# Kernel tuning notes

Hardware: AMD Instinct MI355X
Metric: run time of the kernel (lower is better)

Reference implementation:

```python
import jax, jax.numpy as jnp
import numpy as np

B, S, D = 2, 4096, 1024
H, HD = 16, 64
M = 512              # memseqlen == chunk size
L = 2 * M            # memory + chunk tokens
HID = 2816
EPS = 1e-5


def setup_inputs() -> dict:
    key = jax.random.key(0)
    ks = jax.random.split(key, 16)
    sc = 0.02
    return {
        "x": jax.random.normal(ks[0], (B, S, D), jnp.float32),
        "freqs_cos": jax.random.uniform(ks[1], (L, HD // 2), jnp.float32),
        "freqs_sin": jax.random.uniform(ks[2], (L, HD // 2), jnp.float32),
        "wq": jax.random.normal(ks[3], (D, D), jnp.float32) * sc,
        "wk": jax.random.normal(ks[4], (D, D), jnp.float32) * sc,
        "wv": jax.random.normal(ks[5], (D, D), jnp.float32) * sc,
        "wo": jax.random.normal(ks[6], (D, D), jnp.float32) * sc,
        "wm": jax.random.normal(ks[7], (D, D), jnp.float32) * sc,
        "wkm": jax.random.normal(ks[8], (D, D), jnp.float32) * sc,
        "wvm": jax.random.normal(ks[9], (D, D), jnp.float32) * sc,
        "w1": jax.random.normal(ks[10], (D, HID), jnp.float32) * sc,
        "w3": jax.random.normal(ks[11], (D, HID), jnp.float32) * sc,
        "w2": jax.random.normal(ks[12], (HID, D), jnp.float32) * sc,
        "ffn_norm_w": jnp.ones((D,), jnp.float32),
        "mem_norm_w": jnp.ones((D,), jnp.float32),
        "origin_mem": jnp.zeros((1, M, D), jnp.float32),
    }


def _rmsnorm(x, w):
    return x * jax.lax.rsqrt(jnp.mean(x * x, axis=-1, keepdims=True) + EPS) * w


def _rope(t, cos, sin):
    # t: (B, L, H, HD); cos/sin: (L, HD//2). Adjacent-pair complex rotation (llama2.c style).
    tr = t.reshape(*t.shape[:-1], HD // 2, 2)
    t_r, t_i = tr[..., 0], tr[..., 1]
    c = cos[None, :, None, :]
    s = sin[None, :, None, :]
    o_r = t_r * c - t_i * s
    o_i = t_r * s + t_i * c
    return jnp.stack([o_r, o_i], axis=-1).reshape(t.shape)


def reference(x, freqs_cos, freqs_sin, wq, wk, wv, wo, wm, wkm, wvm,
              w1, w2, w3, ffn_norm_w, mem_norm_w, origin_mem):
    bsz = x.shape[0]
    cos = freqs_cos[:L]
    sin = freqs_sin[:L]
    causal = jnp.tril(jnp.ones((L, L), dtype=bool))
    scale = 1.0 / jnp.sqrt(jnp.asarray(HD, x.dtype))

    def ffn(h):
        return (jax.nn.silu(h @ w1) * (h @ w3)) @ w2

    def step(om, subx):
        # token projections
        xq = (subx @ wq).reshape(bsz, M, H, HD)
        xk = (subx @ wk).reshape(bsz, M, H, HD)
        xv = (subx @ wv).reshape(bsz, M, H, HD)
        # memory glue: wm -> ffn residual -> rmsnorm
        om2 = om @ wm
        om2 = om2 + ffn(_rmsnorm(om2, ffn_norm_w))
        om2 = _rmsnorm(om2, mem_norm_w)
        # memory projections (source bug: mq is overwritten by mk; wqm unused)
        mk = (om2 @ wkm).reshape(bsz, M, H, HD)
        mv = (om2 @ wvm).reshape(bsz, M, H, HD)
        mq = mk
        q = jnp.concatenate([mq, xq], axis=1)  # (B, L, H, HD)
        k = jnp.concatenate([mk, xk], axis=1)
        v = jnp.concatenate([mv, xv], axis=1)
        q = _rope(q, cos, sin)
        k = _rope(k, cos, sin)
        # SDPA, causal over the concatenated length (n_rep == 1, repeat_kv is identity)
        qh = q.transpose(0, 2, 1, 3)
        kh = k.transpose(0, 2, 1, 3)
        vh = v.transpose(0, 2, 1, 3)
        scores = jnp.einsum('bhqd,bhkd->bhqk', qh, kh) * scale
        scores = jnp.where(causal, scores, jnp.finfo(scores.dtype).min)
        attn = jax.nn.softmax(scores, axis=-1)
        out = jnp.einsum('bhqk,bhkd->bhqd', attn, vh)
        out = out.transpose(0, 2, 1, 3).reshape(bsz, L, D)
        om_new = out[:, M:]  # token-part becomes next memory AND this chunk's output
        return om_new, om_new

    om0 = jnp.broadcast_to(origin_mem, (bsz, M, D))
    xc = x.reshape(bsz, S // M, M, D).transpose(1, 0, 2, 3)  # (n_chunks, B, M, D)
    _, outs = jax.lax.scan(step, om0, xc)
    out = outs.transpose(1, 0, 2, 3).reshape(bsz, S, D)
    return out @ wo
```

## Files before the change

kernel.cpp:

```cpp
#include <hip/hip_runtime.h>
#include <hip/hip_bf16.h>


#define D_    1024
#define H_    16
#define HD_   64
#define M_    512
#define L_    1024
#define HID_  2816
#define NSTEP 8

typedef __hip_bfloat16 bf16;
typedef _Float16 f16;
typedef __attribute__((ext_vector_type(8))) short short8;
typedef __attribute__((ext_vector_type(8))) _Float16 f16x8;
typedef __attribute__((ext_vector_type(2))) _Float16 f16x2;
typedef __attribute__((ext_vector_type(4))) float floatx4;

__global__ void probe_dtype(const void* x, int* flag) {
  int lane = threadIdx.x;
  unsigned short v = ((const unsigned short*)x)[2 * lane];
  int e = (v >> 7) & 0xFF;
  bool sane = (e >= 100 && e <= 140);
  unsigned long long m = __ballot(sane);
  if (lane == 0) flag[0] = (__popcll(m) >= 40) ? 1 : 0;
}

__device__ __forceinline__ float load_any(const void* p, long i, int isbf) {
  return isbf ? __bfloat162float(((const bf16*)p)[i]) : ((const float*)p)[i];
}

__global__ __launch_bounds__(256) void transpose_cast(const void* in, bf16* out,
                                                      int K, int N, const int* flagp,
                                                      int stride, int off) {
  __shared__ float tile[32][33];
  int isbf = flagp[0];
  int tx = threadIdx.x & 31, ty = threadIdx.x >> 5;
  int n = blockIdx.x * 32 + tx;
#pragma unroll
  for (int i = 0; i < 4; i++) {
    int k = blockIdx.y * 32 + ty + i * 8;
    tile[ty + i * 8][tx] = load_any(in, (long)k * N + n, isbf);
  }
  __syncthreads();
  int k2 = blockIdx.y * 32 + tx;
#pragma unroll
  for (int i = 0; i < 4; i++) {
    int n2 = blockIdx.x * 32 + ty + i * 8;
    out[((long)n2 * stride + off) * K + k2] = __float2bfloat16(tile[tx][ty + i * 8]);
  }
}

__global__ __launch_bounds__(256) void cast_to_bf16(const void* in, bf16* out, int n,
                                                    const int* flagp) {
  int i = blockIdx.x * 256 + threadIdx.x;
  if (i < n) out[i] = __float2bfloat16(load_any(in, i, flagp[0]));
}

__global__ __launch_bounds__(256) void cast_to_f32(const void* in, float* out, int n,
                                                   const int* flagp) {
  int i = blockIdx.x * 256 + threadIdx.x;
  if (i < n) out[i] = load_any(in, i, flagp[0]);
}

__global__ __launch_bounds__(256) void init_om(const void* in, bf16* om, const int* flagp) {
  int i = blockIdx.x * 256 + threadIdx.x;
  int rem = i & (M_ * D_ - 1);
  om[i] = __float2bfloat16(load_any(in, rem, flagp[0]));
}

__global__ __launch_bounds__(256) void gemm64(
    const bf16* __restrict__ A, const bf16* __restrict__ WT,
    void* __restrict__ out, const int* __restrict__ flagp,
    int N, int K, int out_mode) {
  __shared__ char smem[16384];
  char* aT = smem;
  char* bT = smem + 8192;
  int tid = threadIdx.x;
  int C0 = blockIdx.x * 64, R0 = blockIdx.y * 64;
  int wave = tid >> 6, lane = tid & 63;
  int wm_ = wave >> 1, wn_ = wave & 1;
  floatx4 acc[2][2] = {};

  int q0 = tid, q1 = tid + 256;
  int am0 = q0 >> 3, ac0 = q0 & 7;
  int am1 = q1 >> 3, ac1 = q1 & 7;
  long grow0 = R0 + am0, grow1 = R0 + am1;
  long bn0 = (long)(C0 + am0) * K, bn1 = (long)(C0 + am1) * K;
  int lofa0 = (am0 * 8 + (ac0 ^ (am0 & 7))) * 16;
  int lofa1 = (am1 * 8 + (ac1 ^ (am1 & 7))) * 16;

  for (int k0 = 0; k0 < K; k0 += 64) {
    uint4 va0 = *(const uint4*)(A + grow0 * K + k0 + ac0 * 8);
    uint4 va1 = *(const uint4*)(A + grow1 * K + k0 + ac1 * 8);
    uint4 vb0 = *(const uint4*)(WT + bn0 + k0 + ac0 * 8);
    uint4 vb1 = *(const uint4*)(WT + bn1 + k0 + ac1 * 8);
    __syncthreads();
    *(uint4*)(aT + lofa0) = va0;
    *(uint4*)(aT + lofa1) = va1;
    *(uint4*)(bT + lofa0) = vb0;
    *(uint4*)(bT + lofa1) = vb1;
    __syncthreads();
#pragma unroll
    for (int kki = 0; kki < 2; ++kki) {
      int cbase = kki * 4 + (lane >> 4);
      short8 af[2], bfr[2];
#pragma unroll
      for (int i = 0; i < 2; ++i) {
        int ml = wm_ * 32 + i * 16 + (lane & 15);
        af[i] = *(const short8*)(aT + (ml * 8 + (cbase ^ (ml & 7))) * 16);
        int nl = wn_ * 32 + i * 16 + (lane & 15);
        bfr[i] = *(const short8*)(bT + (nl * 8 + (cbase ^ (nl & 7))) * 16);
      }
#pragma unroll
      for (int i = 0; i < 2; ++i)
#pragma unroll
        for (int j = 0; j < 2; ++j)
          acc[i][j] = __builtin_amdgcn_mfma_f32_16x16x32_bf16(af[i], bfr[j], acc[i][j], 0, 0, 0);
    }
  }
  int isbf = flagp[0];
#pragma unroll
  for (int i = 0; i < 2; ++i)
#pragma unroll
    for (int j = 0; j < 2; ++j) {
      int row = R0 + wm_ * 32 + i * 16 + (lane >> 4) * 4;
      int col = C0 + wn_ * 32 + j * 16 + (lane & 15);
#pragma unroll
      for (int rg = 0; rg < 4; ++rg) {
        float v = acc[i][j][rg];
        long off = (long)(row + rg) * N + col;
        if (out_mode == 0) ((float*)out)[off] = v;
        else if (out_mode == 1) ((f16*)out)[off] = (f16)v;
        else {
          if (isbf) ((bf16*)out)[off] = __float2bfloat16(v);
          else ((float*)out)[off] = v;
        }
      }
    }
}

__global__ __launch_bounds__(256) void gemm64_sk(
    const bf16* __restrict__ A, const bf16* __restrict__ WT,
    float* __restrict__ out0, float* __restrict__ out1,
    int N, int Kfull, int Ksplit) {
  __shared__ char smem[16384];
  char* aT = smem;
  char* bT = smem + 8192;
  int tid = threadIdx.x;
  int C0 = blockIdx.x * 64, R0 = blockIdx.y * 64;
  int kb = blockIdx.z;
  float* out = kb ? out1 : out0;
  int kbeg = kb * Ksplit, kend = kbeg + Ksplit;
  int wave = tid >> 6, lane = tid & 63;
  int wm_ = wave >> 1, wn_ = wave & 1;
  floatx4 acc[2][2] = {};

  int q0 = tid, q1 = tid + 256;
  int am0 = q0 >> 3, ac0 = q0 & 7;
  int am1 = q1 >> 3, ac1 = q1 & 7;
  long grow0 = R0 + am0, grow1 = R0 + am1;
  long bn0 = (long)(C0 + am0) * Kfull, bn1 = (long)(C0 + am1) * Kfull;
  int lofa0 = (am0 * 8 + (ac0 ^ (am0 & 7))) * 16;
  int lofa1 = (am1 * 8 + (ac1 ^ (am1 & 7))) * 16;

  for (int k0 = kbeg; k0 < kend; k0 += 64) {
    uint4 va0 = *(const uint4*)(A + grow0 * Kfull + k0 + ac0 * 8);
    uint4 va1 = *(const uint4*)(A + grow1 * Kfull + k0 + ac1 * 8);
    uint4 vb0 = *(const uint4*)(WT + bn0 + k0 + ac0 * 8);
    uint4 vb1 = *(const uint4*)(WT + bn1 + k0 + ac1 * 8);
    __syncthreads();
    *(uint4*)(aT + lofa0) = va0;
    *(uint4*)(aT + lofa1) = va1;
    *(uint4*)(bT + lofa0) = vb0;
    *(uint4*)(bT + lofa1) = vb1;
    __syncthreads();
#pragma unroll
    for (int kki = 0; kki < 2; ++kki) {
      int cbase = kki * 4 + (lane >> 4);
      short8 af[2], bfr[2];
#pragma unroll
      for (int i = 0; i < 2; ++i) {
        int ml = wm_ * 32 + i * 16 + (lane & 15);
        af[i] = *(const short8*)(aT + (ml * 8 + (cbase ^ (ml & 7))) * 16);
        int nl = wn_ * 32 + i * 16 + (lane & 15);
        bfr[i] = *(const short8*)(bT + (nl * 8 + (cbase ^ (nl & 7))) * 16);
      }
#pragma unroll
      for (int i = 0; i < 2; ++i)
#pragma unroll
        for (int j = 0; j < 2; ++j)
          acc[i][j] = __builtin_amdgcn_mfma_f32_16x16x32_bf16(af[i], bfr[j], acc[i][j], 0, 0, 0);
    }
  }
#pragma unroll
  for (int i = 0; i < 2; ++i)
#pragma unroll
    for (int j = 0; j < 2; ++j) {
      int row = R0 + wm_ * 32 + i * 16 + (lane >> 4) * 4;
      int col = C0 + wn_ * 32 + j * 16 + (lane & 15);
#pragma unroll
      for (int rg = 0; rg < 4; ++rg)
        out[(long)(row + rg) * N + col] = acc[i][j][rg];
    }
}

__global__ __launch_bounds__(256) void gemm128(
    const bf16* __restrict__ A, const bf16* __restrict__ WT,
    void* __restrict__ out, const int* __restrict__ flagp,
    int N, int K, int out_mode) {
  __shared__ char smem[32768];
  int tid = threadIdx.x;
  int w = tid >> 6, lane = tid & 63;
  int C0 = blockIdx.x * 128, R0 = blockIdx.y * 128;
  int wm = (w >> 1) * 64, wn = (w & 1) * 64;
  int g = lane >> 4, n16 = lane & 15;
  floatx4 acc[4][4] = {};
  int lr = lane >> 3, lc = lane & 7;

  for (int k0 = 0; k0 < K; k0 += 64) {
    __syncthreads();
#pragma unroll
    for (int i = 0; i < 4; ++i) {
      int m = w * 32 + i * 8 + lr;
      int cg = lc ^ (m & 7);
      const bf16* ga = A + (size_t)(R0 + m) * K + k0 + cg * 8;
      const bf16* gb = WT + (size_t)(C0 + m) * K + k0 + cg * 8;
      __builtin_amdgcn_global_load_lds(
          (const __attribute__((address_space(1))) void*)ga,
          (__attribute__((address_space(3))) void*)(smem + (w * 32 + i * 8) * 128),
          16, 0, 0);
      __builtin_amdgcn_global_load_lds(
          (const __attribute__((address_space(1))) void*)gb,
          (__attribute__((address_space(3))) void*)(smem + 16384 + (w * 32 + i * 8) * 128),
          16, 0, 0);
    }
    __syncthreads();
#pragma unroll
    for (int kk = 0; kk < 2; ++kk) {
      short8 af[4], bfr[4];
#pragma unroll
      for (int i = 0; i < 4; ++i) {
        int ml = wm + i * 16 + n16;
        af[i] = *(const short8*)(smem + (ml * 8 + ((kk * 4 + g) ^ (ml & 7))) * 16);
        int nl = wn + i * 16 + n16;
        bfr[i] = *(const short8*)(smem + 16384 + (nl * 8 + ((kk * 4 + g) ^ (nl & 7))) * 16);
      }
#pragma unroll
      for (int i = 0; i < 4; ++i)
#pragma unroll
        for (int j = 0; j < 4; ++j)
          acc[i][j] = __builtin_amdgcn_mfma_f32_16x16x32_bf16(af[i], bfr[j], acc[i][j], 0, 0, 0);
    }
  }
  int isbf = flagp[0];
#pragma unroll
  for (int i = 0; i < 4; ++i)
#pragma unroll
    for (int j = 0; j < 4; ++j) {
      int row = R0 + wm + i * 16 + g * 4;
      int col = C0 + wn + j * 16 + n16;
#pragma unroll
      for (int rg = 0; rg < 4; ++rg) {
        float v = acc[i][j][rg];
        if (out_mode == 3) {
          float partner = __shfl_xor(v, 1);
          if ((n16 & 1) == 0) {
            float a = v;
            float s = a / (1.f + __expf(-a));
            ((bf16*)out)[(long)(row + rg) * HID_ + (col >> 1)] =
                __float2bfloat16(s * partner);
          }
          continue;
        }
        long off = (long)(row + rg) * N + col;
        if (out_mode == 0) ((float*)out)[off] = v;
        else if (out_mode == 1) ((f16*)out)[off] = (f16)v;
        else {
          if (isbf) ((bf16*)out)[off] = __float2bfloat16(v);
          else ((float*)out)[off] = v;
        }
      }
    }
}

__global__ __launch_bounds__(256) void rmsnorm_cast(const float* __restrict__ X,
                                                    const float* __restrict__ Wn,
                                                    bf16* __restrict__ Y,
                                                    const float* __restrict__ X1,
                                                    const float* __restrict__ X2,
                                                    float* __restrict__ sumout) {
  int row = blockIdx.x, tid = threadIdx.x;
  const float* xr = X + (long)row * D_;
  float vals[4], ss = 0.f;
#pragma unroll
  for (int i = 0; i < 4; i++) {
    int c = tid + i * 256;
    float v = xr[c];
    if (X1) v += X1[(long)row * D_ + c];
    if (X2) v += X2[(long)row * D_ + c];
    vals[i] = v;
    ss += v * v;
  }
#pragma unroll
  for (int off = 32; off; off >>= 1) ss += __shfl_xor(ss, off);
  __shared__ float wsum[4];
  int wv = tid >> 6, lane = tid & 63;
  if (lane == 0) wsum[wv] = ss;
  __syncthreads();
  ss = wsum[0] + wsum[1] + wsum[2] + wsum[3];
  float r = rsqrtf(ss * (1.0f / D_) + 1e-5f);
#pragma unroll
  for (int i = 0; i < 4; i++) {
    int c = tid + i * 256;
    if (sumout) sumout[(long)row * D_ + c] = vals[i];
    Y[(long)row * D_ + c] = __float2bfloat16(vals[i] * r * Wn[c]);
  }
}

__global__ __launch_bounds__(256) void rope_x(
    const f16* __restrict__ qkv, const float* __restrict__ cosf,
    const float* __restrict__ sinf, f16* __restrict__ q_x,
    f16* __restrict__ k_x, f16* __restrict__ v_xT) {
  __shared__ f16 tile[64][72];
  int pt = blockIdx.x;
  int t = blockIdx.y;
  int bh = blockIdx.z;
  int b = bh >> 4, h = bh & 15;
  int tid = threadIdx.x;
  int i = tid & 31, p0 = tid >> 5;
  size_t slab = (size_t)t * 32 + bh;
#pragma unroll
  for (int j = 0; j < 8; ++j) {
    int pl = p0 + j * 8;
    int m = pt * 64 + pl;
    int pos = 512 + m;
    long base = ((long)b * 4096 + t * 512 + m) * 3072 + h * 64 + 2 * i;
    float c = cosf[pos * 32 + i], s = sinf[pos * 32 + i];
    float q0 = (float)qkv[base], q1 = (float)qkv[base + 1];
    f16x2 qw; qw.x = (f16)((q0 * c - q1 * s) * 0.125f);
    qw.y = (f16)((q0 * s + q1 * c) * 0.125f);
    *(f16x2*)(q_x + (slab * 512 + m) * 64 + 2 * i) = qw;
    float k0 = (float)qkv[base + 1024], k1 = (float)qkv[base + 1025];
    f16x2 kw; kw.x = (f16)(k0 * c - k1 * s); kw.y = (f16)(k0 * s + k1 * c);
    *(f16x2*)(k_x + (slab * 512 + m) * 64 + 2 * i) = kw;
    tile[2 * i][pl] = qkv[base + 2048];
    tile[2 * i + 1][pl] = qkv[base + 2049];
  }
  __syncthreads();
#pragma unroll
  for (int j = 0; j < 8; ++j) {
    int d = p0 + j * 8;
    f16x2 vv; vv.x = tile[d][2 * i]; vv.y = tile[d][2 * i + 1];
    *(f16x2*)(v_xT + (slab * 64 + d) * 512 + pt * 64 + 2 * i) = vv;
  }
}

__global__ __launch_bounds__(256) void rope_mem(
    const f16* __restrict__ mkv, const float* __restrict__ cosf,
    const float* __restrict__ sinf, f16* __restrict__ k_mem,
    f16* __restrict__ v_memT) {
  __shared__ f16 tile[64][72];
  int pt = blockIdx.x;
  int bh = blockIdx.y;
  int b = bh >> 4, h = bh & 15;
  int tid = threadIdx.x;
  int i = tid & 31, p0 = tid >> 5;
#pragma unroll
  for (int j = 0; j < 8; ++j) {
    int pl = p0 + j * 8;
    int pos = pt * 64 + pl;
    long base = ((long)(b * 512 + pos)) * 2048 + h * 64 + 2 * i;
    float c = cosf[pos * 32 + i], s = sinf[pos * 32 + i];
    float k0 = (float)mkv[base], k1 = (float)mkv[base + 1];
    f16x2 kw; kw.x = (f16)(k0 * c - k1 * s); kw.y = (f16)(k0 * s + k1 * c);
    *(f16x2*)(k_mem + ((size_t)bh * 512 + pos) * 64 + 2 * i) = kw;
    tile[2 * i][pl] = mkv[base + 1024];
    tile[2 * i + 1][pl] = mkv[base + 1025];
  }
  __syncthreads();
#pragma unroll
  for (int j = 0; j < 8; ++j) {
    int d = p0 + j * 8;
    f16x2 vv; vv.x = tile[d][2 * i]; vv.y = tile[d][2 * i + 1];
    *(f16x2*)(v_memT + ((size_t)bh * 64 + d) * 512 + pt * 64 + 2 * i) = vv;
  }
}

__global__ __launch_bounds__(256) void attn_mfma(
    const f16* __restrict__ q_x, const f16* __restrict__ k_mem,
    const f16* __restrict__ v_memT, const f16* __restrict__ k_x,
    const f16* __restrict__ v_xT, bf16* __restrict__ om_bf,
    bf16* __restrict__ outs_bf, int t) {
  __shared__ char smem[24576];
  int qt = blockIdx.x, bh = blockIdx.y;
  int tid = threadIdx.x;
  int w = tid >> 6, lane = tid & 63;
  int g = lane >> 4, n16 = lane & 15;
  int numc = 9 + qt;
  int pos = 512 + qt * 64 + w * 16 + n16;
  size_t slab = (size_t)t * 32 + bh;

  f16x8 qf[2];
  {
    const f16* qp = q_x + (slab * 512 + qt * 64 + w * 16 + n16) * 64 + g * 8;
    qf[0] = *(const f16x8*)(qp);
    qf[1] = *(const f16x8*)(qp + 32);
  }
  floatx4 O[4] = {};
  float mrun = -1e30f, lrun = 0.f;

  int id0 = tid, id1 = tid + 256;
  int r0 = id0 >> 3, c0 = id0 & 7;
  int r1 = id1 >> 3, c1 = id1 & 7;
  int lof0 = ((r0 << 3) | (c0 ^ (r0 & 7))) * 16;
  int lof1 = ((r1 << 3) | (c1 ^ (r1 & 7))) * 16;

  auto kaddr = [&](int c, int r) -> const f16* {
    return (c < 8) ? k_mem + ((size_t)bh * 512 + c * 64 + r) * 64
                   : k_x + (slab * 512 + (c - 8) * 64 + r) * 64;
  };
  auto vaddr = [&](int c, int d) -> const f16* {
    return (c < 8) ? v_memT + ((size_t)bh * 64 + d) * 512 + c * 64
                   : v_xT + (slab * 64 + d) * 512 + (c - 8) * 64;
  };

  uint4 kv0 = *(const uint4*)(kaddr(0, r0) + c0 * 8);
  uint4 kv1 = *(const uint4*)(kaddr(0, r1) + c1 * 8);
  uint4 vv0 = *(const uint4*)(vaddr(0, r0) + c0 * 8);
  uint4 vv1 = *(const uint4*)(vaddr(0, r1) + c1 * 8);

  char* Pw = smem + 16384 + w * 2048;

  for (int c = 0; c < numc; ++c) {
    __syncthreads();
    *(uint4*)(smem + lof0) = kv0;
    *(uint4*)(smem + lof1) = kv1;
    *(uint4*)(smem + 8192 + lof0) = vv0;
    *(uint4*)(smem + 8192 + lof1) = vv1;
    if (c + 1 < numc) {
      kv0 = *(const uint4*)(kaddr(c + 1, r0) + c0 * 8);
      kv1 = *(const uint4*)(kaddr(c + 1, r1) + c1 * 8);
      vv0 = *(const uint4*)(vaddr(c + 1, r0) + c0 * 8);
      vv1 = *(const uint4*)(vaddr(c + 1, r1) + c1 * 8);
    }
    __syncthreads();

    floatx4 S[4] = {};
#pragma unroll
    for (int kk = 0; kk < 2; ++kk) {
#pragma unroll
      for (int tn = 0; tn < 4; ++tn) {
        int row = tn * 16 + n16;
        f16x8 kf = *(const f16x8*)(smem + (((row << 3) | ((kk * 4 + g) ^ (row & 7))) * 16));
        S[tn] = __builtin_amdgcn_mfma_f32_16x16x32_f16(kf, qf[kk], S[tn], 0, 0, 0);
      }
    }
    if (c == numc - 1) {
      int kb = 512 + (c - 8) * 64;
#pragma unroll
      for (int tn = 0; tn < 4; ++tn)
#pragma unroll
        for (int r = 0; r < 4; ++r) {
          int key = kb + tn * 16 + g * 4 + r;
          if (key > pos) S[tn][r] = -1e30f;
        }
    }
    float smax = -1e30f;
#pragma unroll
    for (int tn = 0; tn < 4; ++tn)
#pragma unroll
      for (int r = 0; r < 4; ++r) smax = fmaxf(smax, S[tn][r]);
    smax = fmaxf(smax, __shfl_xor(smax, 16));
    smax = fmaxf(smax, __shfl_xor(smax, 32));
    float newm = fmaxf(mrun, smax);
    float corr = __expf(mrun - newm);
    mrun = newm;
    float lsum = 0.f;
    f16 pv[16];
#pragma unroll
    for (int tn = 0; tn < 4; ++tn)
#pragma unroll
      for (int r = 0; r < 4; ++r) {
        float p = __expf(S[tn][r] - newm);
        lsum += p;
        pv[tn * 4 + r] = (f16)p;
      }
    lsum += __shfl_xor(lsum, 16);
    lsum += __shfl_xor(lsum, 32);
    lrun = lrun * corr + lsum;
    float cr[4];
#pragma unroll
    for (int r = 0; r < 4; ++r) cr[r] = __shfl(corr, g * 4 + r);
#pragma unroll
    for (int dt = 0; dt < 4; ++dt)
#pragma unroll
      for (int r = 0; r < 4; ++r) O[dt][r] *= cr[r];
#pragma unroll
    for (int tn = 0; tn < 4; ++tn)
#pragma unroll
      for (int r = 0; r < 4; ++r) {
        int kap = tn * 16 + g * 4 + r;
        *(f16*)(Pw + (((n16 << 3) | ((kap >> 3) ^ (n16 & 7))) * 16 + (kap & 7) * 2)) =
            pv[tn * 4 + r];
      }
#pragma unroll
    for (int kk = 0; kk < 2; ++kk) {
      f16x8 pf = *(const f16x8*)(Pw + (((n16 << 3) | ((kk * 4 + g) ^ (n16 & 7))) * 16));
#pragma unroll
      for (int dt = 0; dt < 4; ++dt) {
        int row = dt * 16 + n16;
        f16x8 vf =
            *(const f16x8*)(smem + 8192 + (((row << 3) | ((kk * 4 + g) ^ (row & 7))) * 16));
        O[dt] = __builtin_amdgcn_mfma_f32_16x16x32_f16(pf, vf, O[dt], 0, 0, 0);
      }
    }
  }
  float rl = 1.0f / lrun;
  float rlr[4];
#pragma unroll
  for (int r = 0; r < 4; ++r) rlr[r] = __shfl(rl, g * 4 + r);
  int b = bh >> 4, h = bh & 15;
#pragma unroll
  for (int dt = 0; dt < 4; ++dt)
#pragma unroll
    for (int r = 0; r < 4; ++r) {
      int qq = qt * 64 + w * 16 + g * 4 + r;
      bf16 v = __float2bfloat16(O[dt][r] * rlr[r]);
      size_t col = h * 64 + dt * 16 + n16;
      om_bf[((size_t)(b * 512 + qq)) * 1024 + col] = v;
      outs_bf[((size_t)(b * 4096 + t * 512 + qq)) * 1024 + col] = v;
    }
}

extern "C" void kernel_launch(void* const* d_in, const int* in_sizes, int n_in,
                              void* d_out, int out_size, void* d_ws, size_t ws_size,
                              hipStream_t stream) {
  (void)in_sizes; (void)n_in; (void)out_size; (void)ws_size;
  const void* x   = d_in[0];
  const void* fc  = d_in[1];
  const void* fs  = d_in[2];
  const void* wq  = d_in[3];
  const void* wk  = d_in[4];
  const void* wv  = d_in[5];
  const void* wo  = d_in[6];
  const void* wm  = d_in[7];
  const void* wkm = d_in[8];
  const void* wvm = d_in[9];
  const void* w1  = d_in[10];
  const void* w3  = d_in[11];
  const void* w2  = d_in[12];
  const void* fnw = d_in[13];
  const void* mnw = d_in[14];
  const void* om0 = d_in[15];

  char* p = (char*)d_ws;
  auto alloc = [&](size_t bytes) -> char* {
    char* r = p;
    p += (bytes + 255) & ~(size_t)255;
    return r;
  };
  int*   flag    = (int*)alloc(256);
  bf16*  wqkvT   = (bf16*)alloc((size_t)3 * 1048576 * 2);
  bf16*  wmT     = (bf16*)alloc((size_t)1048576 * 2);
  bf16*  wkmvmT  = (bf16*)alloc((size_t)2 * 1048576 * 2);
  bf16*  w13T    = (bf16*)alloc((size_t)2 * 2883584 * 2);
  bf16*  w2T     = (bf16*)alloc((size_t)2883584 * 2);
  bf16*  woT     = (bf16*)alloc((size_t)1048576 * 2);
  bf16*  xb      = (bf16*)alloc((size_t)8388608 * 2);
  float* cosf    = (float*)alloc((size_t)32768 * 4);
  float* sinf    = (float*)alloc((size_t)32768 * 4);
  float* ffnw    = (float*)alloc((size_t)1024 * 4);
  float* memw    = (float*)alloc((size_t)1024 * 4);
  bf16*  om_bf   = (bf16*)alloc((size_t)1048576 * 2);
  bf16*  outs_bf = (bf16*)alloc((size_t)8388608 * 2);
  f16*   q_x     = (f16*)alloc((size_t)8 * 32 * 512 * 64 * 2);
  f16*   k_x     = (f16*)alloc((size_t)8 * 32 * 512 * 64 * 2);
  f16*   v_xT    = (f16*)alloc((size_t)8 * 32 * 512 * 64 * 2);
  char*  shr     = alloc((size_t)8192 * 3072 * 2);
  f16*   qkvf_all = (f16*)shr;
  char*  lp = shr;
  auto lalloc = [&](size_t bytes) -> char* {
    char* r = lp;
    lp += (bytes + 255) & ~(size_t)255;
    return r;
  };
  float* om2a   = (float*)lalloc((size_t)1048576 * 4);
  bf16*  h_bf   = (bf16*)lalloc((size_t)1048576 * 2);
  bf16*  u_bf   = (bf16*)lalloc((size_t)2883584 * 2);
  float* fbuf   = (float*)lalloc((size_t)1048576 * 4);
  float* fbuf2  = (float*)lalloc((size_t)1048576 * 4);
  bf16*  om2_bf = (bf16*)lalloc((size_t)1048576 * 2);
  f16*   mkv    = (f16*)lalloc((size_t)2097152 * 2);
  f16*   k_mem  = (f16*)lalloc((size_t)1048576 * 2);
  f16*   v_memT = (f16*)lalloc((size_t)1048576 * 2);

  dim3 tb(256);
  probe_dtype<<<1, 64, 0, stream>>>(x, flag);

  transpose_cast<<<dim3(32, 32), tb, 0, stream>>>(wq, wqkvT, 1024, 1024, flag, 1, 0);
  transpose_cast<<<dim3(32, 32), tb, 0, stream>>>(wk, wqkvT + 1048576, 1024, 1024, flag, 1, 0);
  transpose_cast<<<dim3(32, 32), tb, 0, stream>>>(wv, wqkvT + 2 * 1048576, 1024, 1024, flag, 1, 0);
  transpose_cast<<<dim3(32, 32), tb, 0, stream>>>(wm, wmT, 1024, 1024, flag, 1, 0);
  transpose_cast<<<dim3(32, 32), tb, 0, stream>>>(wkm, wkmvmT, 1024, 1024, flag, 1, 0);
  transpose_cast<<<dim3(32, 32), tb, 0, stream>>>(wvm, wkmvmT + 1048576, 1024, 1024, flag, 1, 0);
  transpose_cast<<<dim3(88, 32), tb, 0, stream>>>(w1, w13T, 1024, 2816, flag, 2, 0);
  transpose_cast<<<dim3(88, 32), tb, 0, stream>>>(w3, w13T, 1024, 2816, flag, 2, 1);
  transpose_cast<<<dim3(32, 88), tb, 0, stream>>>(w2, w2T, 2816, 1024, flag, 1, 0);
  transpose_cast<<<dim3(32, 32), tb, 0, stream>>>(wo, woT, 1024, 1024, flag, 1, 0);

  cast_to_bf16<<<32768, tb, 0, stream>>>(x, xb, 8388608, flag);
  cast_to_f32<<<128, tb, 0, stream>>>(fc, cosf, 32768, flag);
  cast_to_f32<<<128, tb, 0, stream>>>(fs, sinf, 32768, flag);
  cast_to_f32<<<4, tb, 0, stream>>>(fnw, ffnw, 1024, flag);
  cast_to_f32<<<4, tb, 0, stream>>>(mnw, memw, 1024, flag);
  init_om<<<4096, tb, 0, stream>>>(om0, om_bf, flag);

  gemm128<<<dim3(24, 64), tb, 0, stream>>>(xb, wqkvT, qkvf_all, flag, 3072, 1024, 1);
  rope_x<<<dim3(8, 8, 32), tb, 0, stream>>>(qkvf_all, cosf, sinf, q_x, k_x, v_xT);

  for (int t = 0; t < NSTEP; ++t) {
    gemm64_sk<<<dim3(16, 16, 2), tb, 0, stream>>>(om_bf, wmT, om2a, fbuf, 1024, 1024, 512);
    rmsnorm_cast<<<1024, tb, 0, stream>>>(om2a, ffnw, h_bf, fbuf, nullptr, om2a);
    gemm128<<<dim3(44, 8), tb, 0, stream>>>(h_bf, w13T, u_bf, flag, 5632, 1024, 3);
    gemm64_sk<<<dim3(16, 16, 2), tb, 0, stream>>>(u_bf, w2T, fbuf, fbuf2, 1024, 2816, 1408);
    rmsnorm_cast<<<1024, tb, 0, stream>>>(om2a, memw, om2_bf, fbuf, fbuf2, nullptr);
    gemm64<<<dim3(32, 16), tb, 0, stream>>>(om2_bf, wkmvmT, mkv, flag, 2048, 1024, 1);
    rope_mem<<<dim3(8, 32), tb, 0, stream>>>(mkv, cosf, sinf, k_mem, v_memT);
    attn_mfma<<<dim3(8, 32), tb, 0, stream>>>(q_x, k_mem, v_memT, k_x, v_xT,
                                              om_bf, outs_bf, t);
  }
  gemm128<<<dim3(8, 64), tb, 0, stream>>>(outs_bf, woT, d_out, flag, 1024, 1024, 2);
}
```

Before: 1.150 ms.

## Split attention over memory/token keys, fuse RoPE into KV GEMM, swizzle tiles

Attention is split along the key axis into a memory part and a token part, run as two blocks per query tile, and merged by a new kernel that combines the partial softmax statistics. This doubles the number of attention workgroups so a small grid fills more of the GPU. RoPE and the V transpose are folded into the memory K/V GEMM epilogue, which removes the separate rope_mem pass and its intermediate buffer. gemm128 gains an XCD-style block-index swizzle, and s_setprio is raised around the MFMA sections. The cost is an extra fp32 partial-output round trip and one more launch per step.

```diff
diff --git a/kernel.cpp b/kernel.cpp
--- a/kernel.cpp
+++ b/kernel.cpp
@@ -69,56 +69,54 @@
   om[i] = __float2bfloat16(load_any(in, rem, flagp[0]));
 }
 
+#define GEMM64_BODY(Aptr, WTptr, Kld, kbeg, kend)                                   \
+  __shared__ char smem[16384];                                                      \
+  char* aT = smem;                                                                  \
+  char* bT = smem + 8192;                                                           \
+  int tid = threadIdx.x;                                                            \
+  int wave = tid >> 6, lane = tid & 63;                                             \
+  int wm_ = wave >> 1, wn_ = wave & 1;                                              \
+  floatx4 acc[2][2] = {};                                                           \
+  int q0 = tid, q1 = tid + 256;                                                     \
+  int am0 = q0 >> 3, ac0 = q0 & 7;                                                  \
+  int am1 = q1 >> 3, ac1 = q1 & 7;                                                  \
+  long grow0 = R0 + am0, grow1 = R0 + am1;                                          \
+  long bn0 = (long)(C0 + am0) * (Kld), bn1 = (long)(C0 + am1) * (Kld);              \
+  int lofa0 = (am0 * 8 + (ac0 ^ (am0 & 7))) * 16;                                   \
+  int lofa1 = (am1 * 8 + (ac1 ^ (am1 & 7))) * 16;                                   \
+  for (int k0 = (kbeg); k0 < (kend); k0 += 64) {                                    \
+    uint4 va0 = *(const uint4*)((Aptr) + grow0 * (Kld) + k0 + ac0 * 8);             \
+    uint4 va1 = *(const uint4*)((Aptr) + grow1 * (Kld) + k0 + ac1 * 8);             \
+    uint4 vb0 = *(const uint4*)((WTptr) + bn0 + k0 + ac0 * 8);                      \
+    uint4 vb1 = *(const uint4*)((WTptr) + bn1 + k0 + ac1 * 8);                      \
+    __syncthreads();                                                                \
+    *(uint4*)(aT + lofa0) = va0;                                                    \
+    *(uint4*)(aT + lofa1) = va1;                                                    \
+    *(uint4*)(bT + lofa0) = vb0;                                                    \
+    *(uint4*)(bT + lofa1) = vb1;                                                    \
+    __syncthreads();                                                                \
+    _Pragma("unroll") for (int kki = 0; kki < 2; ++kki) {                           \
+      int cbase = kki * 4 + (lane >> 4);                                            \
+      short8 af[2], bfr[2];                                                         \
+      _Pragma("unroll") for (int i = 0; i < 2; ++i) {                               \
+        int ml = wm_ * 32 + i * 16 + (lane & 15);                                   \
+        af[i] = *(const short8*)(aT + (ml * 8 + (cbase ^ (ml & 7))) * 16);          \
+        int nl = wn_ * 32 + i * 16 + (lane & 15);                                   \
+        bfr[i] = *(const short8*)(bT + (nl * 8 + (cbase ^ (nl & 7))) * 16);         \
+      }                                                                             \
+      _Pragma("unroll") for (int i = 0; i < 2; ++i)                                 \
+          _Pragma("unroll") for (int j = 0; j < 2; ++j) acc[i][j] =                 \
+              __builtin_amdgcn_mfma_f32_16x16x32_bf16(af[i], bfr[j], acc[i][j],     \
+                                                      0, 0, 0);                     \
+    }                                                                               \
+  }
+
 __global__ __launch_bounds__(256) void gemm64(
     const bf16* __restrict__ A, const bf16* __restrict__ WT,
     void* __restrict__ out, const int* __restrict__ flagp,
     int N, int K, int out_mode) {
-  __shared__ char smem[16384];
-  char* aT = smem;
-  char* bT = smem + 8192;
-  int tid = threadIdx.x;
   int C0 = blockIdx.x * 64, R0 = blockIdx.y * 64;
-  int wave = tid >> 6, lane = tid & 63;
-  int wm_ = wave >> 1, wn_ = wave & 1;
-  floatx4 acc[2][2] = {};
-
-  int q0 = tid, q1 = tid + 256;
-  int am0 = q0 >> 3, ac0 = q0 & 7;
-  int am1 = q1 >> 3, ac1 = q1 & 7;
-  long grow0 = R0 + am0, grow1 = R0 + am1;
-  long bn0 = (long)(C0 + am0) * K, bn1 = (long)(C0 + am1) * K;
-  int lofa0 = (am0 * 8 + (ac0 ^ (am0 & 7))) * 16;
-  int lofa1 = (am1 * 8 + (ac1 ^ (am1 & 7))) * 16;
-
-  for (int k0 = 0; k0 < K; k0 += 64) {
-    uint4 va0 = *(const uint4*)(A + grow0 * K + k0 + ac0 * 8);
-    uint4 va1 = *(const uint4*)(A + grow1 * K + k0 + ac1 * 8);
-    uint4 vb0 = *(const uint4*)(WT + bn0 + k0 + ac0 * 8);
-    uint4 vb1 = *(const uint4*)(WT + bn1 + k0 + ac1 * 8);
-    __syncthreads();
-    *(uint4*)(aT + lofa0) = va0;
-    *(uint4*)(aT + lofa1) = va1;
-    *(uint4*)(bT + lofa0) = vb0;
-    *(uint4*)(bT + lofa1) = vb1;
-    __syncthreads();
-#pragma unroll
-    for (int kki = 0; kki < 2; ++kki) {
-      int cbase = kki * 4 + (lane >> 4);
-      short8 af[2], bfr[2];
-#pragma unroll
-      for (int i = 0; i < 2; ++i) {
-        int ml = wm_ * 32 + i * 16 + (lane & 15);
-        af[i] = *(const short8*)(aT + (ml * 8 + (cbase ^ (ml & 7))) * 16);
-        int nl = wn_ * 32 + i * 16 + (lane & 15);
-        bfr[i] = *(const short8*)(bT + (nl * 8 + (cbase ^ (nl & 7))) * 16);
-      }
-#pragma unroll
-      for (int i = 0; i < 2; ++i)
-#pragma unroll
-        for (int j = 0; j < 2; ++j)
-          acc[i][j] = __builtin_amdgcn_mfma_f32_16x16x32_bf16(af[i], bfr[j], acc[i][j], 0, 0, 0);
-    }
-  }
+  GEMM64_BODY(A, WT, K, 0, K)
   int isbf = flagp[0];
 #pragma unroll
   for (int i = 0; i < 2; ++i)
@@ -144,55 +142,11 @@
     const bf16* __restrict__ A, const bf16* __restrict__ WT,
     float* __restrict__ out0, float* __restrict__ out1,
     int N, int Kfull, int Ksplit) {
-  __shared__ char smem[16384];
-  char* aT = smem;
-  char* bT = smem + 8192;
-  int tid = threadIdx.x;
   int C0 = blockIdx.x * 64, R0 = blockIdx.y * 64;
   int kb = blockIdx.z;
   float* out = kb ? out1 : out0;
-  int kbeg = kb * Ksplit, kend = kbeg + Ksplit;
-  int wave = tid >> 6, lane = tid & 63;
-  int wm_ = wave >> 1, wn_ = wave & 1;
-  floatx4 acc[2][2] = {};
-
-  int q0 = tid, q1 = tid + 256;
-  int am0 = q0 >> 3, ac0 = q0 & 7;
-  int am1 = q1 >> 3, ac1 = q1 & 7;
-  long grow0 = R0 + am0, grow1 = R0 + am1;
-  long bn0 = (long)(C0 + am0) * Kfull, bn1 = (long)(C0 + am1) * Kfull;
-  int lofa0 = (am0 * 8 + (ac0 ^ (am0 & 7))) * 16;
-  int lofa1 = (am1 * 8 + (ac1 ^ (am1 & 7))) * 16;
-
-  for (int k0 = kbeg; k0 < kend; k0 += 64) {
-    uint4 va0 = *(const uint4*)(A + grow0 * Kfull + k0 + ac0 * 8);
-    uint4 va1 = *(const uint4*)(A + grow1 * Kfull + k0 + ac1 * 8);
-    uint4 vb0 = *(const uint4*)(WT + bn0 + k0 + ac0 * 8);
-    uint4 vb1 = *(const uint4*)(WT + bn1 + k0 + ac1 * 8);
-    __syncthreads();
-    *(uint4*)(aT + lofa0) = va0;
-    *(uint4*)(aT + lofa1) = va1;
-    *(uint4*)(bT + lofa0) = vb0;
-    *(uint4*)(bT + lofa1) = vb1;
-    __syncthreads();
-#pragma unroll
-    for (int kki = 0; kki < 2; ++kki) {
-      int cbase = kki * 4 + (lane >> 4);
-      short8 af[2], bfr[2];
-#pragma unroll
-      for (int i = 0; i < 2; ++i) {
-        int ml = wm_ * 32 + i * 16 + (lane & 15);
-        af[i] = *(const short8*)(aT + (ml * 8 + (cbase ^ (ml & 7))) * 16);
-        int nl = wn_ * 32 + i * 16 + (lane & 15);
-        bfr[i] = *(const short8*)(bT + (nl * 8 + (cbase ^ (nl & 7))) * 16);
-      }
-#pragma unroll
-      for (int i = 0; i < 2; ++i)
-#pragma unroll
-        for (int j = 0; j < 2; ++j)
-          acc[i][j] = __builtin_amdgcn_mfma_f32_16x16x32_bf16(af[i], bfr[j], acc[i][j], 0, 0, 0);
-    }
-  }
+  int kbeg = kb * Ksplit;
+  GEMM64_BODY(A, WT, Kfull, kbeg, kbeg + Ksplit)
 #pragma unroll
   for (int i = 0; i < 2; ++i)
 #pragma unroll
@@ -202,6 +156,39 @@
 #pragma unroll
       for (int rg = 0; rg < 4; ++rg)
         out[(long)(row + rg) * N + col] = acc[i][j][rg];
+    }
+}
+
+__global__ __launch_bounds__(256) void gemm64_kmvm(
+    const bf16* __restrict__ A, const bf16* __restrict__ WT,
+    const float* __restrict__ cosf, const float* __restrict__ sinf,
+    f16* __restrict__ k_mem, f16* __restrict__ v_memT) {
+  int C0 = blockIdx.x * 64, R0 = blockIdx.y * 64;
+  GEMM64_BODY(A, WT, 1024, 0, 1024)
+#pragma unroll
+  for (int i = 0; i < 2; ++i)
+#pragma unroll
+    for (int j = 0; j < 2; ++j) {
+      int row0 = R0 + wm_ * 32 + i * 16 + (lane >> 4) * 4;
+      int col = C0 + wn_ * 32 + j * 16 + (lane & 15);
+#pragma unroll
+      for (int rg = 0; rg < 4; ++rg) {
+        float v = acc[i][j][rg];
+        int row = row0 + rg;
+        int b = row >> 9, pos = row & 511;
+        if (C0 < 1024) {
+          float partner = __shfl_xor(v, 1);
+          int ii = (col & 63) >> 1;
+          float c = cosf[pos * 32 + ii], s = sinf[pos * 32 + ii];
+          float o = (col & 1) ? (partner * s + v * c) : (v * c - partner * s);
+          int bh = b * 16 + ((col >> 6) & 15);
+          k_mem[((size_t)bh * 512 + pos) * 64 + (col & 63)] = (f16)o;
+        } else {
+          int d = col & 63;
+          int bh = b * 16 + ((col - 1024) >> 6);
+          v_memT[((size_t)bh * 64 + d) * 512 + pos] = (f16)v;
+        }
+      }
     }
 }
 
@@ -212,7 +199,17 @@
   __shared__ char smem[32768];
   int tid = threadIdx.x;
   int w = tid >> 6, lane = tid & 63;
-  int C0 = blockIdx.x * 128, R0 = blockIdx.y * 128;
+  int bx = blockIdx.x, by = blockIdx.y;
+  {
+    int nwg = gridDim.x * gridDim.y;
+    if ((nwg & 7) == 0) {
+      int lin = by * gridDim.x + bx;
+      int swz = (lin & 7) * (nwg >> 3) + (lin >> 3);
+      bx = swz % gridDim.x;
+      by = swz / gridDim.x;
+    }
+  }
+  int C0 = bx * 128, R0 = by * 128;
   int wm = (w >> 1) * 64, wn = (w & 1) * 64;
   int g = lane >> 4, n16 = lane & 15;
   floatx4 acc[4][4] = {};
@@ -356,48 +353,18 @@
   }
 }
 
-__global__ __launch_bounds__(256) void rope_mem(
-    const f16* __restrict__ mkv, const float* __restrict__ cosf,
-    const float* __restrict__ sinf, f16* __restrict__ k_mem,
-    f16* __restrict__ v_memT) {
-  __shared__ f16 tile[64][72];
-  int pt = blockIdx.x;
-  int bh = blockIdx.y;
-  int b = bh >> 4, h = bh & 15;
-  int tid = threadIdx.x;
-  int i = tid & 31, p0 = tid >> 5;
-#pragma unroll
-  for (int j = 0; j < 8; ++j) {
-    int pl = p0 + j * 8;
-    int pos = pt * 64 + pl;
-    long base = ((long)(b * 512 + pos)) * 2048 + h * 64 + 2 * i;
-    float c = cosf[pos * 32 + i], s = sinf[pos * 32 + i];
-    float k0 = (float)mkv[base], k1 = (float)mkv[base + 1];
-    f16x2 kw; kw.x = (f16)(k0 * c - k1 * s); kw.y = (f16)(k0 * s + k1 * c);
-    *(f16x2*)(k_mem + ((size_t)bh * 512 + pos) * 64 + 2 * i) = kw;
-    tile[2 * i][pl] = mkv[base + 1024];
-    tile[2 * i + 1][pl] = mkv[base + 1025];
-  }
-  __syncthreads();
-#pragma unroll
-  for (int j = 0; j < 8; ++j) {
-    int d = p0 + j * 8;
-    f16x2 vv; vv.x = tile[d][2 * i]; vv.y = tile[d][2 * i + 1];
-    *(f16x2*)(v_memT + ((size_t)bh * 64 + d) * 512 + pt * 64 + 2 * i) = vv;
-  }
-}
-
 __global__ __launch_bounds__(256) void attn_mfma(
     const f16* __restrict__ q_x, const f16* __restrict__ k_mem,
     const f16* __restrict__ v_memT, const f16* __restrict__ k_x,
-    const f16* __restrict__ v_xT, bf16* __restrict__ om_bf,
-    bf16* __restrict__ outs_bf, int t) {
+    const f16* __restrict__ v_xT, float* __restrict__ Opart,
+    float* __restrict__ mpart, float* __restrict__ lpart, int t) {
   __shared__ char smem[24576];
-  int qt = blockIdx.x, bh = blockIdx.y;
+  int qt = blockIdx.x, bh = blockIdx.y, z = blockIdx.z;
   int tid = threadIdx.x;
   int w = tid >> 6, lane = tid & 63;
   int g = lane >> 4, n16 = lane & 15;
-  int numc = 9 + qt;
+  int c0 = z ? 8 : 0;
+  int numc = z ? (qt + 1) : 8;
   int pos = 512 + qt * 64 + w * 16 + n16;
   size_t slab = (size_t)t * 32 + bh;
 
@@ -411,10 +378,10 @@
   float mrun = -1e30f, lrun = 0.f;
 
   int id0 = tid, id1 = tid + 256;
-  int r0 = id0 >> 3, c0 = id0 & 7;
-  int r1 = id1 >> 3, c1 = id1 & 7;
-  int lof0 = ((r0 << 3) | (c0 ^ (r0 & 7))) * 16;
-  int lof1 = ((r1 << 3) | (c1 ^ (r1 & 7))) * 16;
+  int r0 = id0 >> 3, cc0 = id0 & 7;
+  int r1 = id1 >> 3, cc1 = id1 & 7;
+  int lof0 = ((r0 << 3) | (cc0 ^ (r0 & 7))) * 16;
+  int lof1 = ((r1 << 3) | (cc1 ^ (r1 & 7))) * 16;
 
   auto kaddr = [&](int c, int r) -> const f16* {
     return (c < 8) ? k_mem + ((size_t)bh * 512 + c * 64 + r) * 64
@@ -425,10 +392,10 @@
                    : v_xT + (slab * 64 + d) * 512 + (c - 8) * 64;
   };
 
-  uint4 kv0 = *(const uint4*)(kaddr(0, r0) + c0 * 8);
-  uint4 kv1 = *(const uint4*)(kaddr(0, r1) + c1 * 8);
-  uint4 vv0 = *(const uint4*)(vaddr(0, r0) + c0 * 8);
-  uint4 vv1 = *(const uint4*)(vaddr(0, r1) + c1 * 8);
+  uint4 kv0 = *(const uint4*)(kaddr(c0, r0) + cc0 * 8);
+  uint4 kv1 = *(const uint4*)(kaddr(c0, r1) + cc1 * 8);
+  uint4 vv0 = *(const uint4*)(vaddr(c0, r0) + cc0 * 8);
+  uint4 vv1 = *(const uint4*)(vaddr(c0, r1) + cc1 * 8);
 
   char* Pw = smem + 16384 + w * 2048;
 
@@ -439,14 +406,15 @@
     *(uint4*)(smem + 8192 + lof0) = vv0;
     *(uint4*)(smem + 8192 + lof1) = vv1;
     if (c + 1 < numc) {
-      kv0 = *(const uint4*)(kaddr(c + 1, r0) + c0 * 8);
-      kv1 = *(const uint4*)(kaddr(c + 1, r1) + c1 * 8);
-      vv0 = *(const uint4*)(vaddr(c + 1, r0) + c0 * 8);
-      vv1 = *(const uint4*)(vaddr(c + 1, r1) + c1 * 8);
+      kv0 = *(const uint4*)(kaddr(c0 + c + 1, r0) + cc0 * 8);
+      kv1 = *(const uint4*)(kaddr(c0 + c + 1, r1) + cc1 * 8);
+      vv0 = *(const uint4*)(vaddr(c0 + c + 1, r0) + cc0 * 8);
+      vv1 = *(const uint4*)(vaddr(c0 + c + 1, r1) + cc1 * 8);
     }
     __syncthreads();
 
     floatx4 S[4] = {};
+    __builtin_amdgcn_s_setprio(1);
 #pragma unroll
     for (int kk = 0; kk < 2; ++kk) {
 #pragma unroll
@@ -456,8 +424,9 @@
         S[tn] = __builtin_amdgcn_mfma_f32_16x16x32_f16(kf, qf[kk], S[tn], 0, 0, 0);
       }
     }
-    if (c == numc - 1) {
-      int kb = 512 + (c - 8) * 64;
+    __builtin_amdgcn_s_setprio(0);
+    if (z == 1 && c == numc - 1) {
+      int kb = 512 + qt * 64;
 #pragma unroll
       for (int tn = 0; tn < 4; ++tn)
 #pragma unroll
@@ -504,6 +473,7 @@
         *(f16*)(Pw + (((n16 << 3) | ((kap >> 3) ^ (n16 & 7))) * 16 + (kap & 7) * 2)) =
             pv[tn * 4 + r];
       }
+    __builtin_amdgcn_s_setprio(1);
 #pragma unroll
     for (int kk = 0; kk < 2; ++kk) {
       f16x8 pf = *(const f16x8*)(Pw + (((n16 << 3) | ((kk * 4 + g) ^ (n16 & 7))) * 16));
@@ -515,22 +485,47 @@
         O[dt] = __builtin_amdgcn_mfma_f32_16x16x32_f16(pf, vf, O[dt], 0, 0, 0);
       }
     }
-  }
-  float rl = 1.0f / lrun;
-  float rlr[4];
-#pragma unroll
-  for (int r = 0; r < 4; ++r) rlr[r] = __shfl(rl, g * 4 + r);
+    __builtin_amdgcn_s_setprio(0);
+  }
   int b = bh >> 4, h = bh & 15;
+  if (g == 0) {
+    int qq = qt * 64 + w * 16 + n16;
+    mpart[(size_t)z * 16384 + bh * 512 + qq] = mrun;
+    lpart[(size_t)z * 16384 + bh * 512 + qq] = lrun;
+  }
 #pragma unroll
   for (int dt = 0; dt < 4; ++dt)
 #pragma unroll
     for (int r = 0; r < 4; ++r) {
       int qq = qt * 64 + w * 16 + g * 4 + r;
-      bf16 v = __float2bfloat16(O[dt][r] * rlr[r]);
-      size_t col = h * 64 + dt * 16 + n16;
-      om_bf[((size_t)(b * 512 + qq)) * 1024 + col] = v;
-      outs_bf[((size_t)(b * 4096 + t * 512 + qq)) * 1024 + col] = v;
-    }
+      size_t col = (size_t)h * 64 + dt * 16 + n16;
+      Opart[(size_t)z * 1048576 + (size_t)(b * 512 + qq) * 1024 + col] = O[dt][r];
+    }
+}
+
+__global__ __launch_bounds__(256) void attn_merge(
+    const float* __restrict__ Opart, const float* __restrict__ mpart,
+    const float* __restrict__ lpart, bf16* __restrict__ om_bf,
+    bf16* __restrict__ outs_bf, int t) {
+  int row = blockIdx.x;
+  int b = row >> 9, qq = row & 511;
+  int tid = threadIdx.x;
+#pragma unroll
+  for (int ii = 0; ii < 4; ++ii) {
+    int col = tid + ii * 256;
+    int bh = b * 16 + (col >> 6);
+    int idx = bh * 512 + qq;
+    float m1 = mpart[idx], l1 = lpart[idx];
+    float m2 = mpart[16384 + idx], l2 = lpart[16384 + idx];
+    float Mx = fmaxf(m1, m2);
+    float a1 = __expf(m1 - Mx), a2 = __expf(m2 - Mx);
+    float o1 = Opart[(size_t)row * 1024 + col];
+    float o2 = Opart[1048576 + (size_t)row * 1024 + col];
+    float v = (a1 * o1 + a2 * o2) / (a1 * l1 + a2 * l2);
+    bf16 bv = __float2bfloat16(v);
+    om_bf[(size_t)row * 1024 + col] = bv;
+    outs_bf[((size_t)(b * 4096 + t * 512 + qq)) * 1024 + col] = bv;
+  }
 }
 
 extern "C" void kernel_launch(void* const* d_in, const int* in_sizes, int n_in,
@@ -591,9 +586,11 @@
   float* fbuf   = (float*)lalloc((size_t)1048576 * 4);
   float* fbuf2  = (float*)lalloc((size_t)1048576 * 4);
   bf16*  om2_bf = (bf16*)lalloc((size_t)1048576 * 2);
-  f16*   mkv    = (f16*)lalloc((size_t)2097152 * 2);
   f16*   k_mem  = (f16*)lalloc((size_t)1048576 * 2);
   f16*   v_memT = (f16*)lalloc((size_t)1048576 * 2);
+  float* Opart  = (float*)lalloc((size_t)2 * 1048576 * 4);
+  float* mpart  = (float*)lalloc((size_t)2 * 16384 * 4);
+  float* lpart  = (float*)lalloc((size_t)2 * 16384 * 4);
 
   dim3 tb(256);
   probe_dtype<<<1, 64, 0, stream>>>(x, flag);
@@ -625,10 +622,10 @@
     gemm128<<<dim3(44, 8), tb, 0, stream>>>(h_bf, w13T, u_bf, flag, 5632, 1024, 3);
     gemm64_sk<<<dim3(16, 16, 2), tb, 0, stream>>>(u_bf, w2T, fbuf, fbuf2, 1024, 2816, 1408);
     rmsnorm_cast<<<1024, tb, 0, stream>>>(om2a, memw, om2_bf, fbuf, fbuf2, nullptr);
-    gemm64<<<dim3(32, 16), tb, 0, stream>>>(om2_bf, wkmvmT, mkv, flag, 2048, 1024, 1);
-    rope_mem<<<dim3(8, 32), tb, 0, stream>>>(mkv, cosf, sinf, k_mem, v_memT);
-    attn_mfma<<<dim3(8, 32), tb, 0, stream>>>(q_x, k_mem, v_memT, k_x, v_xT,
-                                              om_bf, outs_bf, t);
+    gemm64_kmvm<<<dim3(32, 16), tb, 0, stream>>>(om2_bf, wkmvmT, cosf, sinf, k_mem, v_memT);
+    attn_mfma<<<dim3(8, 32, 2), tb, 0, stream>>>(q_x, k_mem, v_memT, k_x, v_xT,
+                                                 Opart, mpart, lpart, t);
+    attn_merge<<<1024, tb, 0, stream>>>(Opart, mpart, lpart, om_bf, outs_bf, t);
   }
   gemm128<<<dim3(8, 64), tb, 0, stream>>>(outs_bf, woT, d_out, flag, 1024, 1024, 2);
 }
```

Result: no change. 1.140 ms (-0.9%).
